# Optimization experiments

Measured on AMD Instinct MI355X. Metric: run time of the kernel, lower is better.

The kernel has to match this reference:

```python
import jax, jax.numpy as jnp
import numpy as np

TOPK = 10  # self.k in the module
EPS = 1e-8

def setup_inputs() -> dict:
    key = jax.random.key(0)
    ks = jax.random.split(key, 7)
    B, H, S, D = 4, 16, 2048, 64
    M = 1000  # memory_size
    hidden = H * D
    return {
        "inputs": jax.random.normal(ks[0], (B, S, hidden), dtype=jnp.float32),
        "q": jax.random.normal(ks[1], (B, H, S, D), dtype=jnp.float32),
        "k": jax.random.normal(ks[2], (B, H, S, D), dtype=jnp.float32),
        "v": jax.random.normal(ks[3], (B, H, S, D), dtype=jnp.float32),
        "attention_mask": jnp.ones((B, S), dtype=jnp.float32),
        "mem_keys": jax.random.normal(ks[4], (M, hidden), dtype=jnp.float32),
        "mem_values": jax.random.normal(ks[5], (M, hidden), dtype=jnp.float32),
        "mem_positions": jnp.arange(M, dtype=jnp.float32),
        "seq_len_q": S,
    }


def reference(inputs, q, k, v, attention_mask, mem_keys, mem_values, mem_positions, seq_len_q):
    B, H, S, D = q.shape
    # positions_q: token_indices is None -> arange per batch
    positions_q = jnp.broadcast_to(jnp.arange(S, dtype=jnp.float32)[None, :], (B, S))
    # query key: last-position key across heads, flattened -> [B, H*D]
    query_key = jnp.transpose(k[:, :, -1, :], (0, 1, 2)).reshape(B, H * D)
    # cosine similarity against memory bank [M, H*D]
    qn = query_key / (jnp.linalg.norm(query_key, axis=-1, keepdims=True) + EPS)
    mn = mem_keys / (jnp.linalg.norm(mem_keys, axis=-1, keepdims=True) + EPS)
    sims = jnp.einsum("bh,mh->bm", qn, mn)  # [B, M]
    _, top_idx = jax.lax.top_k(sims, TOPK)  # [B, K]
    # gather retrieved events
    r_k = mem_keys[top_idx]        # [B, K, H*D]
    r_v = mem_values[top_idx]      # [B, K, H*D]
    r_pos = mem_positions[top_idx]  # [B, K]
    # reshape to per-head tokens: [B, H, K, D]
    r_k = r_k.reshape(B, TOPK, H, D).transpose(0, 2, 1, 3)
    r_v = r_v.reshape(B, TOPK, H, D).transpose(0, 2, 1, 3)
    # prepend retrieved tokens along the key/value sequence axis
    k_aug = jnp.concatenate([r_k, k], axis=2)  # [B, H, K+S, D]
    v_aug = jnp.concatenate([r_v, v], axis=2)
    mask_aug = jnp.concatenate(
        [jnp.ones((B, TOPK), dtype=attention_mask.dtype), attention_mask], axis=1)
    positions_k = jnp.concatenate([positions_q, r_pos], axis=1)  # [B, S+K]
    seq_len_k = S + TOPK
    return inputs, q, k_aug, v_aug, mask_aug, seq_len_k, positions_k
```

## Files before the change

### kernel.cpp

```cpp
#include <hip/hip_runtime.h>

#define B 4
#define H 16
#define S 2048
#define D 64
#define M 1000
#define TOPKN 10
#define HID 1024

#define O4E 33636352U
#define O5E 33644584U
#define O6E 33644585U
#define O2C 4194304U
#define O3C 6301696U
#define BHSTR 32928U
#define CF 2097152U
#define T4C (4u * CF)

#define NSIMS 125
#define NCOPYBLK 1923
#define NTH (NCOPYBLK * 256u)

__device__ __forceinline__ void chunk_src_dst(
    unsigned int c, const float4* __restrict__ s0,
    const float4* __restrict__ s1, const float4* __restrict__ s2,
    const float4* __restrict__ s3, float4& val, unsigned int& dst) {
  if (c < CF) {
    val = s0[c];
    dst = c;
  } else if (c < 2u * CF) {
    val = s1[c - CF];
    dst = c;
  } else {
    bool isv = (c >= 3u * CF);
    unsigned int idx = c - (isv ? 3u : 2u) * CF;
    unsigned int bh = idx >> 15;
    unsigned int r = idx & 32767u;
    dst = (isv ? O3C : O2C) + bh * BHSTR + 160u + r;
    val = (isv ? s3 : s2)[idx];
  }
}

__global__ __launch_bounds__(256) void fused_stage1(
    const float* __restrict__ in0, const float* __restrict__ qin,
    const float* __restrict__ kin, const float* __restrict__ vin,
    const float* __restrict__ mkeys, float* __restrict__ out,
    float* __restrict__ ws, unsigned int outElems) {
  const int blk = blockIdx.x;
  const int tid = threadIdx.x;

  __shared__ float4 s_q4[B][256];
  __shared__ float s_qn[B];

  if (blk >= NSIMS) {
    const unsigned int outChunks = outElems >> 2;
    const float4* s0 = (const float4*)in0;
    const float4* s1 = (const float4*)qin;
    const float4* s2 = (const float4*)kin;
    const float4* s3 = (const float4*)vin;
    float4* o = (float4*)out;
    unsigned int c = (unsigned int)(blk - NSIMS) * 256u + (unsigned int)tid;
    while (c + 3u * NTH < T4C) {
      float4 v0, v1, v2, v3;
      unsigned int d0, d1, d2, d3;
      chunk_src_dst(c, s0, s1, s2, s3, v0, d0);
      chunk_src_dst(c + NTH, s0, s1, s2, s3, v1, d1);
      chunk_src_dst(c + 2u * NTH, s0, s1, s2, s3, v2, d2);
      chunk_src_dst(c + 3u * NTH, s0, s1, s2, s3, v3, d3);
      if (d0 < outChunks) o[d0] = v0;
      if (d1 < outChunks) o[d1] = v1;
      if (d2 < outChunks) o[d2] = v2;
      if (d3 < outChunks) o[d3] = v3;
      c += 4u * NTH;
    }
    for (; c < T4C; c += NTH) {
      float4 v;
      unsigned int d;
      chunk_src_dst(c, s0, s1, s2, s3, v, d);
      if (d < outChunks) o[d] = v;
    }
  } else {
    for (int i = tid; i < B * 256; i += 256) {
      int b = i >> 8, c = i & 255;
      int h = c >> 4, dd = (c & 15) << 2;
      s_q4[b][c] = *(const float4*)(kin +
                                    ((size_t)(b * H + h) * S + (S - 1)) * D +
                                    dd);
    }
    __syncthreads();

    const int lane = tid & 63;
    const int w = tid >> 6;

    {
      float ss = 0.f;
      for (int j = 0; j < 4; ++j) {
        float4 v = s_q4[w][lane + j * 64];
        ss += v.x * v.x + v.y * v.y + v.z * v.z + v.w * v.w;
      }
      for (int off = 32; off; off >>= 1) ss += __shfl_xor(ss, off);
      if (lane == 0) s_qn[w] = sqrtf(ss) + 1e-8f;
    }
    __syncthreads();

    const float4* mk4 = (const float4*)mkeys;
    for (int r = 0; r < 2; ++r) {
      const int m = blk * 8 + w * 2 + r;
      float d0 = 0.f, d1 = 0.f, d2 = 0.f, d3 = 0.f, msq = 0.f;
#pragma unroll
      for (int j = 0; j < 4; ++j) {
        float4 ch = mk4[(size_t)m * 256 + lane + j * 64];
        float4 q0 = s_q4[0][lane + j * 64];
        float4 q1 = s_q4[1][lane + j * 64];
        float4 q2 = s_q4[2][lane + j * 64];
        float4 q3 = s_q4[3][lane + j * 64];
        d0 += q0.x * ch.x + q0.y * ch.y + q0.z * ch.z + q0.w * ch.w;
        d1 += q1.x * ch.x + q1.y * ch.y + q1.z * ch.z + q1.w * ch.w;
        d2 += q2.x * ch.x + q2.y * ch.y + q2.z * ch.z + q2.w * ch.w;
        d3 += q3.x * ch.x + q3.y * ch.y + q3.z * ch.z + q3.w * ch.w;
        msq += ch.x * ch.x + ch.y * ch.y + ch.z * ch.z + ch.w * ch.w;
      }
      for (int off = 32; off; off >>= 1) {
        d0 += __shfl_xor(d0, off);
        d1 += __shfl_xor(d1, off);
        d2 += __shfl_xor(d2, off);
        d3 += __shfl_xor(d3, off);
        msq += __shfl_xor(msq, off);
      }
      if (lane == 0) {
        float den = sqrtf(msq) + 1e-8f;
        ws[0 * 1024 + m] = d0 / (s_qn[0] * den);
        ws[1 * 1024 + m] = d1 / (s_qn[1] * den);
        ws[2 * 1024 + m] = d2 / (s_qn[2] * den);
        ws[3 * 1024 + m] = d3 / (s_qn[3] * den);
      }
    }
  }
}

__global__ __launch_bounds__(256) void fused_stage2(
    const float* __restrict__ amask, const float* __restrict__ mkeys,
    const float* __restrict__ mvals, const float* __restrict__ mpos,
    const float* __restrict__ ws, float* __restrict__ out,
    unsigned int outElems) {
  const int b = blockIdx.x;
  const int tid = threadIdx.x;
  const unsigned int outChunks = outElems >> 2;
  const int SK = S + TOPKN;

  __shared__ float s_sims[1024];
  __shared__ float s_rv[256];
  __shared__ int s_ri[256];
  __shared__ int s_top[TOPKN];

  for (int i = tid; i < 1024; i += 256)
    s_sims[i] = (i < M) ? ws[b * 1024 + i] : -INFINITY;

  for (int i = tid; i < SK; i += 256) {
    unsigned int d4 = O4E + (unsigned int)(b * SK + i);
    if (d4 < outElems)
      out[d4] = (i < TOPKN) ? 1.0f : amask[b * S + (i - TOPKN)];
    unsigned int d6 = O6E + (unsigned int)(b * SK + i);
    if (i < S && d6 < outElems) out[d6] = (float)i;
  }
  if (b == 0 && tid == 0 && O5E < outElems)
    out[O5E] = 2064.0f;
  __syncthreads();

  for (int t = 0; t < TOPKN; ++t) {
    int base = tid * 4;
    float bv = s_sims[base];
    int bi = base;
    for (int j = 1; j < 4; ++j) {
      float v = s_sims[base + j];
      if (v > bv) { bv = v; bi = base + j; }
    }
    s_rv[tid] = bv;
    s_ri[tid] = bi;
    __syncthreads();
    for (int w = 128; w > 0; w >>= 1) {
      if (tid < w) {
        float ov = s_rv[tid + w];
        int oi = s_ri[tid + w];
        if (ov > s_rv[tid] || (ov == s_rv[tid] && oi < s_ri[tid])) {
          s_rv[tid] = ov;
          s_ri[tid] = oi;
        }
      }
      __syncthreads();
    }
    if (tid == 0) {
      int sel = s_ri[0];
      s_sims[sel] = -INFINITY;
      s_top[t] = (sel < M) ? sel : (M - 1);
    }
    __syncthreads();
  }

  if (tid < TOPKN) {
    unsigned int d6 = O6E + (unsigned int)(b * SK + S + tid);
    if (d6 < outElems) out[d6] = mpos[s_top[tid]];
  }

  const float4* mk4 = (const float4*)mkeys;
  const float4* mv4 = (const float4*)mvals;
  float4* o = (float4*)out;
  for (int c = tid; c < 5120; c += 256) {
    int isv = (c >= 2560);
    int cc = isv ? c - 2560 : c;
    int row = cc >> 4, ch = cc & 15;
    int h = row / 10, kk = row - h * 10;
    int im = s_top[kk];
    const float4* src = isv ? mv4 : mk4;
    unsigned int dst = (isv ? O3C : O2C) +
                       (unsigned int)((b * H + h) * BHSTR + kk * 16 + ch);
    if (dst < outChunks) o[dst] = src[(size_t)im * 256 + h * 16 + ch];
  }
}

extern "C" void kernel_launch(void* const* d_in, const int* in_sizes, int n_in,
                              void* d_out, int out_size, void* d_ws, size_t ws_size,
                              hipStream_t stream) {
  const float* in0 = (const float*)d_in[0];
  const float* q   = (const float*)d_in[1];
  const float* k   = (const float*)d_in[2];
  const float* v   = (const float*)d_in[3];
  const float* am  = (const float*)d_in[4];
  const float* mk  = (const float*)d_in[5];
  const float* mv  = (const float*)d_in[6];
  const float* mp  = (const float*)d_in[7];
  (void)in_sizes; (void)n_in; (void)ws_size;

  float* ws = (float*)d_ws;

  fused_stage1<<<NSIMS + NCOPYBLK, 256, 0, stream>>>(
      in0, q, k, v, mk, (float*)d_out, ws, (unsigned int)out_size);
  fused_stage2<<<B, 256, 0, stream>>>(
      am, mk, mv, mp, ws, (float*)d_out, (unsigned int)out_size);
}
```

Baseline: 284.2 us.

## Split fused stage into separate sims and flat-grid copy kernels

Splits the fused first stage into a small similarity kernel and a separate copy kernel, run as three launches on one stream. The copy kernel now uses a flat grid of 8192 blocks, each thread handling four float4 chunks, in place of a grid-stride loop over 1923 blocks. This removes the branch-divergent block roles and the loop overhead. In exchange it adds a launch and loses the overlap of the similarity computation with the copy.

```diff
diff --git a/kernel.cpp b/kernel.cpp
--- a/kernel.cpp
+++ b/kernel.cpp
@@ -15,11 +15,9 @@
 #define O3C 6301696U
 #define BHSTR 32928U
 #define CF 2097152U
-#define T4C (4u * CF)
 
 #define NSIMS 125
-#define NCOPYBLK 1923
-#define NTH (NCOPYBLK * 256u)
+#define NCOPY 8192
 
 __device__ __forceinline__ void chunk_src_dst(
     unsigned int c, const float4* __restrict__ s0,
@@ -41,99 +39,89 @@
   }
 }
 
-__global__ __launch_bounds__(256) void fused_stage1(
+__global__ __launch_bounds__(256) void copy_kernel(
     const float* __restrict__ in0, const float* __restrict__ qin,
     const float* __restrict__ kin, const float* __restrict__ vin,
-    const float* __restrict__ mkeys, float* __restrict__ out,
-    float* __restrict__ ws, unsigned int outElems) {
+    float* __restrict__ out, unsigned int outElems) {
+  const unsigned int outChunks = outElems >> 2;
+  const float4* s0 = (const float4*)in0;
+  const float4* s1 = (const float4*)qin;
+  const float4* s2 = (const float4*)kin;
+  const float4* s3 = (const float4*)vin;
+  float4* o = (float4*)out;
+  unsigned int base = blockIdx.x * 1024u + threadIdx.x;
+#pragma unroll
+  for (int k = 0; k < 4; ++k) {
+    unsigned int c = base + (unsigned int)k * 256u;
+    float4 v;
+    unsigned int d;
+    chunk_src_dst(c, s0, s1, s2, s3, v, d);
+    if (d < outChunks) o[d] = v;
+  }
+}
+
+__global__ __launch_bounds__(256) void sims_kernel(
+    const float* __restrict__ kin, const float* __restrict__ mkeys,
+    float* __restrict__ ws) {
   const int blk = blockIdx.x;
   const int tid = threadIdx.x;
 
   __shared__ float4 s_q4[B][256];
   __shared__ float s_qn[B];
 
-  if (blk >= NSIMS) {
-    const unsigned int outChunks = outElems >> 2;
-    const float4* s0 = (const float4*)in0;
-    const float4* s1 = (const float4*)qin;
-    const float4* s2 = (const float4*)kin;
-    const float4* s3 = (const float4*)vin;
-    float4* o = (float4*)out;
-    unsigned int c = (unsigned int)(blk - NSIMS) * 256u + (unsigned int)tid;
-    while (c + 3u * NTH < T4C) {
-      float4 v0, v1, v2, v3;
-      unsigned int d0, d1, d2, d3;
-      chunk_src_dst(c, s0, s1, s2, s3, v0, d0);
-      chunk_src_dst(c + NTH, s0, s1, s2, s3, v1, d1);
-      chunk_src_dst(c + 2u * NTH, s0, s1, s2, s3, v2, d2);
-      chunk_src_dst(c + 3u * NTH, s0, s1, s2, s3, v3, d3);
-      if (d0 < outChunks) o[d0] = v0;
-      if (d1 < outChunks) o[d1] = v1;
-      if (d2 < outChunks) o[d2] = v2;
-      if (d3 < outChunks) o[d3] = v3;
-      c += 4u * NTH;
-    }
-    for (; c < T4C; c += NTH) {
-      float4 v;
-      unsigned int d;
-      chunk_src_dst(c, s0, s1, s2, s3, v, d);
-      if (d < outChunks) o[d] = v;
-    }
-  } else {
-    for (int i = tid; i < B * 256; i += 256) {
-      int b = i >> 8, c = i & 255;
-      int h = c >> 4, dd = (c & 15) << 2;
-      s_q4[b][c] = *(const float4*)(kin +
-                                    ((size_t)(b * H + h) * S + (S - 1)) * D +
-                                    dd);
-    }
-    __syncthreads();
-
-    const int lane = tid & 63;
-    const int w = tid >> 6;
-
-    {
-      float ss = 0.f;
-      for (int j = 0; j < 4; ++j) {
-        float4 v = s_q4[w][lane + j * 64];
-        ss += v.x * v.x + v.y * v.y + v.z * v.z + v.w * v.w;
-      }
-      for (int off = 32; off; off >>= 1) ss += __shfl_xor(ss, off);
-      if (lane == 0) s_qn[w] = sqrtf(ss) + 1e-8f;
-    }
-    __syncthreads();
-
-    const float4* mk4 = (const float4*)mkeys;
-    for (int r = 0; r < 2; ++r) {
-      const int m = blk * 8 + w * 2 + r;
-      float d0 = 0.f, d1 = 0.f, d2 = 0.f, d3 = 0.f, msq = 0.f;
+  for (int i = tid; i < B * 256; i += 256) {
+    int b = i >> 8, c = i & 255;
+    int h = c >> 4, dd = (c & 15) << 2;
+    s_q4[b][c] = *(const float4*)(kin +
+                                  ((size_t)(b * H + h) * S + (S - 1)) * D +
+                                  dd);
+  }
+  __syncthreads();
+
+  const int lane = tid & 63;
+  const int w = tid >> 6;
+
+  {
+    float ss = 0.f;
+    for (int j = 0; j < 4; ++j) {
+      float4 v = s_q4[w][lane + j * 64];
+      ss += v.x * v.x + v.y * v.y + v.z * v.z + v.w * v.w;
+    }
+    for (int off = 32; off; off >>= 1) ss += __shfl_xor(ss, off);
+    if (lane == 0) s_qn[w] = sqrtf(ss) + 1e-8f;
+  }
+  __syncthreads();
+
+  const float4* mk4 = (const float4*)mkeys;
+  for (int r = 0; r < 2; ++r) {
+    const int m = blk * 8 + w * 2 + r;
+    float d0 = 0.f, d1 = 0.f, d2 = 0.f, d3 = 0.f, msq = 0.f;
 #pragma unroll
-      for (int j = 0; j < 4; ++j) {
-        float4 ch = mk4[(size_t)m * 256 + lane + j * 64];
-        float4 q0 = s_q4[0][lane + j * 64];
-        float4 q1 = s_q4[1][lane + j * 64];
-        float4 q2 = s_q4[2][lane + j * 64];
-        float4 q3 = s_q4[3][lane + j * 64];
-        d0 += q0.x * ch.x + q0.y * ch.y + q0.z * ch.z + q0.w * ch.w;
-        d1 += q1.x * ch.x + q1.y * ch.y + q1.z * ch.z + q1.w * ch.w;
-        d2 += q2.x * ch.x + q2.y * ch.y + q2.z * ch.z + q2.w * ch.w;
-        d3 += q3.x * ch.x + q3.y * ch.y + q3.z * ch.z + q3.w * ch.w;
-        msq += ch.x * ch.x + ch.y * ch.y + ch.z * ch.z + ch.w * ch.w;
-      }
-      for (int off = 32; off; off >>= 1) {
-        d0 += __shfl_xor(d0, off);
-        d1 += __shfl_xor(d1, off);
-        d2 += __shfl_xor(d2, off);
-        d3 += __shfl_xor(d3, off);
-        msq += __shfl_xor(msq, off);
-      }
-      if (lane == 0) {
-        float den = sqrtf(msq) + 1e-8f;
-        ws[0 * 1024 + m] = d0 / (s_qn[0] * den);
-        ws[1 * 1024 + m] = d1 / (s_qn[1] * den);
-        ws[2 * 1024 + m] = d2 / (s_qn[2] * den);
-        ws[3 * 1024 + m] = d3 / (s_qn[3] * den);
-      }
+    for (int j = 0; j < 4; ++j) {
+      float4 ch = mk4[(size_t)m * 256 + lane + j * 64];
+      float4 q0 = s_q4[0][lane + j * 64];
+      float4 q1 = s_q4[1][lane + j * 64];
+      float4 q2 = s_q4[2][lane + j * 64];
+      float4 q3 = s_q4[3][lane + j * 64];
+      d0 += q0.x * ch.x + q0.y * ch.y + q0.z * ch.z + q0.w * ch.w;
+      d1 += q1.x * ch.x + q1.y * ch.y + q1.z * ch.z + q1.w * ch.w;
+      d2 += q2.x * ch.x + q2.y * ch.y + q2.z * ch.z + q2.w * ch.w;
+      d3 += q3.x * ch.x + q3.y * ch.y + q3.z * ch.z + q3.w * ch.w;
+      msq += ch.x * ch.x + ch.y * ch.y + ch.z * ch.z + ch.w * ch.w;
+    }
+    for (int off = 32; off; off >>= 1) {
+      d0 += __shfl_xor(d0, off);
+      d1 += __shfl_xor(d1, off);
+      d2 += __shfl_xor(d2, off);
+      d3 += __shfl_xor(d3, off);
+      msq += __shfl_xor(msq, off);
+    }
+    if (lane == 0) {
+      float den = sqrtf(msq) + 1e-8f;
+      ws[0 * 1024 + m] = d0 / (s_qn[0] * den);
+      ws[1 * 1024 + m] = d1 / (s_qn[1] * den);
+      ws[2 * 1024 + m] = d2 / (s_qn[2] * den);
+      ws[3 * 1024 + m] = d3 / (s_qn[3] * den);
     }
   }
 }
@@ -231,10 +219,12 @@
   const float* mp  = (const float*)d_in[7];
   (void)in_sizes; (void)n_in; (void)ws_size;
 
+  float* out = (float*)d_out;
   float* ws = (float*)d_ws;
 
-  fused_stage1<<<NSIMS + NCOPYBLK, 256, 0, stream>>>(
-      in0, q, k, v, mk, (float*)d_out, ws, (unsigned int)out_size);
-  fused_stage2<<<B, 256, 0, stream>>>(
-      am, mk, mv, mp, ws, (float*)d_out, (unsigned int)out_size);
-}
+  sims_kernel<<<NSIMS, 256, 0, stream>>>(k, mk, ws);
+  copy_kernel<<<NCOPY, 256, 0, stream>>>(in0, q, k, v, out,
+                                         (unsigned int)out_size);
+  fused_stage2<<<B, 256, 0, stream>>>(am, mk, mv, mp, ws, out,
+                                      (unsigned int)out_size);
+}
```

Result: slower. 290.5 us (+2.2%).
